# Kernel optimization log

Measured on AMD Instinct MI355X. Metric: run time of the kernel, lower is better.

The kernel has to match this reference:

```python
import jax, jax.numpy as jnp
import numpy as np

EMB_SCALE = 0.001  # embedding_scale when normalize=False


def setup_inputs() -> dict:
    key = jax.random.key(0)
    k1, k2 = jax.random.split(key)
    N, S, C, V, K = 8, 4096, 2, 128, 512
    x0 = jax.random.normal(k1, (N, S, C, V), dtype=jnp.float32)
    embedding = jax.random.normal(k2, (C, K, V), dtype=jnp.float32) * EMB_SCALE
    return {"x0": x0, "embedding": embedding}


def reference(x0, embedding):
    # normalize=False path: x = x0, embedding used as-is
    N, S, C, V = x0.shape
    K = embedding.shape[1]
    x = x0
    xf = x.reshape(N * S, C, V)  # (B, C, V), B = N*S tokens

    # (the ||x||^2 term is constant over k). Avoids materializing (B, C, K, V).
    dots = jnp.einsum('bcv,ckv->bck', xf, embedding)          # (B, C, K)
    e_sq = jnp.sum(embedding * embedding, axis=2)             # (C, K)
    dist2 = e_sq[None, :, :] - 2.0 * dots                     # (B, C, K)
    index = jnp.argmin(dist2, axis=2)                         # (B, C) int

    # Entropy of codebook usage (original divides by len(index) == B rows)
    B = N * S
    hist = jnp.bincount(index.reshape(-1), length=K).astype(jnp.float32)
    prob = hist / jnp.float32(B)
    entropy = -jnp.sum(jnp.where(hist > 0, prob * jnp.log(jnp.maximum(prob, 1e-30)), 0.0))

    # Gather: output[b, c] = embedding[c, index[b, c]]
    output = embedding[jnp.arange(C), index]                  # (B, C, V)
    output = output.reshape(N, S, C, V)

    out0 = jax.lax.stop_gradient(output - x) + x              # straight-through
    out1 = jnp.sum((jax.lax.stop_gradient(x) - output) ** 2, axis=3)  # (N,S,C)
    out2 = (jnp.sum((x - jax.lax.stop_gradient(output)) ** 2, axis=3)
            + jnp.sum((x - x0) ** 2, axis=3))                 # (N,S,C); (x-x0)==0 here
    return (out0, out1, out2, entropy)
```

## Files before the change

### kernel.cpp

```cpp
#include <hip/hip_runtime.h>
#include <math.h>

#define N_TOK    32768
#define C_CH     2
#define V_DIM    128
#define K_CODES  512
#define TPB      64

typedef short     bf16v8 __attribute__((ext_vector_type(8)));
typedef float     f32x4  __attribute__((ext_vector_type(4)));
typedef unsigned  u32x4  __attribute__((ext_vector_type(4)));

__device__ inline unsigned f2bf(float f) {
    unsigned u = __float_as_uint(f);
    return (u + 0x7FFFu + ((u >> 16) & 1u)) >> 16;
}
__device__ inline unsigned mapf(float d) {
    unsigned u = __float_as_uint(d);
    return ((int)u < 0) ? ~u : (u | 0x80000000u);
}

__device__ inline void pin4(u32x4& v) {
    unsigned a0 = v[0], a1 = v[1], a2 = v[2], a3 = v[3];
    asm volatile("" : "+v"(a0), "+v"(a1), "+v"(a2), "+v"(a3));
    v[0] = a0; v[1] = a1; v[2] = a2; v[3] = a3;
}

__global__ __launch_bounds__(64) void vq_prep(const float* __restrict__ emb,
                                              float* __restrict__ e_sq,
                                              unsigned int* __restrict__ hist,
                                              unsigned char* __restrict__ img) {
    const int row  = blockIdx.x;
    const int lane = threadIdx.x;
    const float a = emb[(size_t)row * V_DIM + lane];
    const float b = emb[(size_t)row * V_DIM + 64 + lane];
    float s = a * a + b * b;
#pragma unroll
    for (int off = 32; off; off >>= 1) s += __shfl_down(s, off);
    if (lane == 0) {
        e_sq[row] = s;
        if (row < K_CODES) hist[row] = 0u;
    }
    if (lane < 16) {
        const float* src = emb + (size_t)row * V_DIM + lane * 8;
        u32x4 val;
#pragma unroll
        for (int q = 0; q < 4; ++q)
            val[q] = f2bf(src[2 * q]) | (f2bf(src[2 * q + 1]) << 16);
        *reinterpret_cast<u32x4*>(img + ((size_t)row * 16 + lane) * 16) = val;
    }
}

__global__ __launch_bounds__(512, 2) void vq_main(const float* __restrict__ x0,
                                                  const float* __restrict__ emb,
                                                  const float* __restrict__ e_sq,
                                                  const unsigned char* __restrict__ img,
                                                  unsigned int* __restrict__ hist,
                                                  float* __restrict__ out0,
                                                  float* __restrict__ out1,
                                                  float* __restrict__ out2) {
    __shared__ unsigned long long best_s[TPB];

    const int c    = blockIdx.y;
    const int gt0  = blockIdx.x * TPB;
    const int t    = threadIdx.x;
    const int lane = t & 63;
    const int w    = t >> 6;
    const int l15  = lane & 15;
    const int l4   = lane >> 4;

    if (t < TPB) best_s[t] = ~0ull;

    u32x4 Bf[4][4];
    {
        const unsigned char* imgc = img + (size_t)(c * K_CODES + w * 64) * 256;
#pragma unroll
        for (int ct = 0; ct < 4; ++ct)
#pragma unroll
            for (int kk = 0; kk < 4; ++kk) {
                Bf[ct][kk] = *reinterpret_cast<const u32x4*>(
                    imgc + (size_t)(ct * 16 + l15) * 256 + (kk * 4 + l4) * 16);
                pin4(Bf[ct][kk]);
            }
    }
    float esq_r[4];
#pragma unroll
    for (int ct = 0; ct < 4; ++ct)
        esq_r[ct] = e_sq[c * K_CODES + w * 64 + ct * 16 + l15];

    __syncthreads();

    f32x4 raw[8];
    auto LOADX = [&](int tile_) {
        const float* xp = x0 + ((size_t)(gt0 + tile_ * 16 + l15) * C_CH + c) * V_DIM
                        + l4 * 8;
#pragma unroll
        for (int kk = 0; kk < 4; ++kk) {
            raw[2 * kk]     = *reinterpret_cast<const f32x4*>(xp + kk * 32);
            raw[2 * kk + 1] = *reinterpret_cast<const f32x4*>(xp + kk * 32 + 4);
        }
    };

    LOADX(0);
#pragma unroll
    for (int tile = 0; tile < 4; ++tile) {
        u32x4 A[4];
#pragma unroll
        for (int kk = 0; kk < 4; ++kk) {
            const f32x4 lo = raw[2 * kk], hi = raw[2 * kk + 1];
            u32x4 v;
            v[0] = f2bf(lo[0]) | (f2bf(lo[1]) << 16);
            v[1] = f2bf(lo[2]) | (f2bf(lo[3]) << 16);
            v[2] = f2bf(hi[0]) | (f2bf(hi[1]) << 16);
            v[3] = f2bf(hi[2]) | (f2bf(hi[3]) << 16);
            A[kk] = v;
        }

        if (tile < 3) LOADX(tile + 1);

        f32x4 acc[4];
#pragma unroll
        for (int ct = 0; ct < 4; ++ct) acc[ct] = (f32x4){0.f, 0.f, 0.f, 0.f};
#pragma unroll
        for (int kk = 0; kk < 4; ++kk)
#pragma unroll
            for (int ct = 0; ct < 4; ++ct)
                acc[ct] = __builtin_amdgcn_mfma_f32_16x16x32_bf16(
                    __builtin_bit_cast(bf16v8, A[kk]),
                    __builtin_bit_cast(bf16v8, Bf[ct][kk]), acc[ct], 0, 0, 0);

#pragma unroll
        for (int r = 0; r < 4; ++r) {
            unsigned long long m = ~0ull;
#pragma unroll
            for (int ct = 0; ct < 4; ++ct) {
                const float d = fmaf(-2.f, acc[ct][r], esq_r[ct]);
                const unsigned long long p =
                    ((unsigned long long)mapf(d) << 32)
                    | (unsigned)(w * 64 + ct * 16 + l15);
                if (p < m) m = p;
            }
#pragma unroll
            for (int s = 1; s < 16; s <<= 1) {
                const unsigned long long o = __shfl_xor(m, s);
                if (o < m) m = o;
            }
            if (l15 == 0)
                atomicMin(&best_s[tile * 16 + l4 * 4 + r], m);
        }
    }
    __syncthreads();

    const int g  = t >> 5;
    const int gl = t & 31;
#pragma unroll
    for (int i = 0; i < 4; ++i) {
        const int tok = i * 16 + g;
        const int k   = (int)(best_s[tok] & (unsigned long long)(K_CODES - 1));
        const size_t rowi = (size_t)(gt0 + tok) * C_CH + c;
        const f32x4 ev = *reinterpret_cast<const f32x4*>(
            emb + ((size_t)c * K_CODES + k) * V_DIM + gl * 4);
        const f32x4 xv = *reinterpret_cast<const f32x4*>(
            x0 + rowi * V_DIM + gl * 4);
        f32x4 ov;
        float s = 0.f;
#pragma unroll
        for (int z = 0; z < 4; ++z) {
            ov[z] = (ev[z] - xv[z]) + xv[z];
            const float dz = xv[z] - ev[z];
            s = fmaf(dz, dz, s);
        }
        *reinterpret_cast<f32x4*>(out0 + rowi * V_DIM + gl * 4) = ov;
#pragma unroll
        for (int m2 = 1; m2 <= 16; m2 <<= 1) s += __shfl_xor(s, m2);
        if (gl == 0) {
            out1[rowi] = s;
            out2[rowi] = s;
            atomicAdd(&hist[k], 1u);
        }
    }
}

__global__ __launch_bounds__(512) void vq_entropy(const unsigned int* __restrict__ hist,
                                                  float* __restrict__ ent) {
    const int t = threadIdx.x;
    float v = 0.f;
    const unsigned int h = hist[t];
    if (h > 0u) {
        const float p = (float)h * (1.0f / 32768.0f);
        v = p * logf(p);
    }
#pragma unroll
    for (int off = 32; off; off >>= 1) v += __shfl_down(v, off);
    __shared__ float s[8];
    if ((t & 63) == 0) s[t >> 6] = v;
    __syncthreads();
    if (t == 0) {
        float tot = 0.f;
#pragma unroll
        for (int i = 0; i < 8; ++i) tot += s[i];
        ent[0] = -tot;
    }
}

extern "C" void kernel_launch(void* const* d_in, const int* in_sizes, int n_in,
                              void* d_out, int out_size, void* d_ws, size_t ws_size,
                              hipStream_t stream) {
    const float* x0  = (const float*)d_in[0];
    const float* emb = (const float*)d_in[1];

    float*         e_sq = (float*)d_ws;
    unsigned int*  hist = (unsigned int*)((char*)d_ws + 4096);
    unsigned char* img  = (unsigned char*)d_ws + 8192;

    float* out0 = (float*)d_out;
    float* out1 = out0 + (size_t)N_TOK * C_CH * V_DIM;
    float* out2 = out1 + (size_t)N_TOK * C_CH;
    float* ent  = out2 + (size_t)N_TOK * C_CH;

    vq_prep<<<C_CH * K_CODES, 64, 0, stream>>>(emb, e_sq, hist, img);
    vq_main<<<dim3(N_TOK / TPB, C_CH), 512, 0, stream>>>(x0, emb, e_sq, img, hist,
                                                         out0, out1, out2);
    vq_entropy<<<1, K_CODES, 0, stream>>>(hist, ent);
}
```

Measured before the change: 88.40 us.

## Keep token tiles in registers and stream codebook fragments per wave

Restructures the distance kernel so each wave keeps two 16-token x tiles as bf16 fragments in registers and streams its 128 codes from the preconverted image in 16-code chunks. Previously each wave pinned 64 codes in registers and looped over four token tiles. The block shrinks from 64 tokens and 512 threads to 32 tokens and 256 threads, doubling the grid and dropping the two-blocks-per-CU launch bound. The intent is lower register pressure and more occupancy. The cost is reloading codebook fragments from global memory or L2 once per block, with less reuse per load.

Result: faster. 83.89 us (-5.1%).

```diff
diff --git a/kernel.cpp b/kernel.cpp
--- a/kernel.cpp
+++ b/kernel.cpp
@@ -5,7 +5,7 @@
 #define C_CH     2
 #define V_DIM    128
 #define K_CODES  512
-#define TPB      64
+#define TPB      32
 
 typedef short     bf16v8 __attribute__((ext_vector_type(8)));
 typedef float     f32x4  __attribute__((ext_vector_type(4)));
@@ -18,12 +18,6 @@
 __device__ inline unsigned mapf(float d) {
     unsigned u = __float_as_uint(d);
     return ((int)u < 0) ? ~u : (u | 0x80000000u);
-}
-
-__device__ inline void pin4(u32x4& v) {
-    unsigned a0 = v[0], a1 = v[1], a2 = v[2], a3 = v[3];
-    asm volatile("" : "+v"(a0), "+v"(a1), "+v"(a2), "+v"(a3));
-    v[0] = a0; v[1] = a1; v[2] = a2; v[3] = a3;
 }
 
 __global__ __launch_bounds__(64) void vq_prep(const float* __restrict__ emb,
@@ -51,14 +45,14 @@
     }
 }
 
-__global__ __launch_bounds__(512, 2) void vq_main(const float* __restrict__ x0,
-                                                  const float* __restrict__ emb,
-                                                  const float* __restrict__ e_sq,
-                                                  const unsigned char* __restrict__ img,
-                                                  unsigned int* __restrict__ hist,
-                                                  float* __restrict__ out0,
-                                                  float* __restrict__ out1,
-                                                  float* __restrict__ out2) {
+__global__ __launch_bounds__(256) void vq_main(const float* __restrict__ x0,
+                                               const float* __restrict__ emb,
+                                               const float* __restrict__ e_sq,
+                                               const unsigned char* __restrict__ img,
+                                               unsigned int* __restrict__ hist,
+                                               float* __restrict__ out0,
+                                               float* __restrict__ out1,
+                                               float* __restrict__ out2) {
     __shared__ unsigned long long best_s[TPB];
 
     const int c    = blockIdx.y;
@@ -71,82 +65,99 @@
 
     if (t < TPB) best_s[t] = ~0ull;
 
-    u32x4 Bf[4][4];
-    {
-        const unsigned char* imgc = img + (size_t)(c * K_CODES + w * 64) * 256;
-#pragma unroll
-        for (int ct = 0; ct < 4; ++ct)
-#pragma unroll
-            for (int kk = 0; kk < 4; ++kk) {
-                Bf[ct][kk] = *reinterpret_cast<const u32x4*>(
-                    imgc + (size_t)(ct * 16 + l15) * 256 + (kk * 4 + l4) * 16);
-                pin4(Bf[ct][kk]);
-            }
-    }
-    float esq_r[4];
-#pragma unroll
-    for (int ct = 0; ct < 4; ++ct)
-        esq_r[ct] = e_sq[c * K_CODES + w * 64 + ct * 16 + l15];
+    u32x4 A0[4], A1[4];
+#pragma unroll
+    for (int kk = 0; kk < 4; ++kk) {
+        const float* xp0 = x0 + ((size_t)(gt0 + l15) * C_CH + c) * V_DIM
+                         + kk * 32 + l4 * 8;
+        const f32x4 lo0 = *reinterpret_cast<const f32x4*>(xp0);
+        const f32x4 hi0 = *reinterpret_cast<const f32x4*>(xp0 + 4);
+        u32x4 v;
+        v[0] = f2bf(lo0[0]) | (f2bf(lo0[1]) << 16);
+        v[1] = f2bf(lo0[2]) | (f2bf(lo0[3]) << 16);
+        v[2] = f2bf(hi0[0]) | (f2bf(hi0[1]) << 16);
+        v[3] = f2bf(hi0[2]) | (f2bf(hi0[3]) << 16);
+        A0[kk] = v;
+    }
+#pragma unroll
+    for (int kk = 0; kk < 4; ++kk) {
+        const float* xp1 = x0 + ((size_t)(gt0 + 16 + l15) * C_CH + c) * V_DIM
+                         + kk * 32 + l4 * 8;
+        const f32x4 lo1 = *reinterpret_cast<const f32x4*>(xp1);
+        const f32x4 hi1 = *reinterpret_cast<const f32x4*>(xp1 + 4);
+        u32x4 v;
+        v[0] = f2bf(lo1[0]) | (f2bf(lo1[1]) << 16);
+        v[1] = f2bf(lo1[2]) | (f2bf(lo1[3]) << 16);
+        v[2] = f2bf(hi1[0]) | (f2bf(hi1[1]) << 16);
+        v[3] = f2bf(hi1[2]) | (f2bf(hi1[3]) << 16);
+        A1[kk] = v;
+    }
+
+    float esq_r[8];
+#pragma unroll
+    for (int j = 0; j < 8; ++j)
+        esq_r[j] = e_sq[c * K_CODES + w * 128 + j * 16 + l15];
 
     __syncthreads();
 
-    f32x4 raw[8];
-    auto LOADX = [&](int tile_) {
-        const float* xp = x0 + ((size_t)(gt0 + tile_ * 16 + l15) * C_CH + c) * V_DIM
-                        + l4 * 8;
-#pragma unroll
-        for (int kk = 0; kk < 4; ++kk) {
-            raw[2 * kk]     = *reinterpret_cast<const f32x4*>(xp + kk * 32);
-            raw[2 * kk + 1] = *reinterpret_cast<const f32x4*>(xp + kk * 32 + 4);
-        }
-    };
-
-    LOADX(0);
-#pragma unroll
-    for (int tile = 0; tile < 4; ++tile) {
-        u32x4 A[4];
-#pragma unroll
-        for (int kk = 0; kk < 4; ++kk) {
-            const f32x4 lo = raw[2 * kk], hi = raw[2 * kk + 1];
-            u32x4 v;
-            v[0] = f2bf(lo[0]) | (f2bf(lo[1]) << 16);
-            v[1] = f2bf(lo[2]) | (f2bf(lo[3]) << 16);
-            v[2] = f2bf(hi[0]) | (f2bf(hi[1]) << 16);
-            v[3] = f2bf(hi[2]) | (f2bf(hi[3]) << 16);
-            A[kk] = v;
-        }
-
-        if (tile < 3) LOADX(tile + 1);
-
-        f32x4 acc[4];
-#pragma unroll
-        for (int ct = 0; ct < 4; ++ct) acc[ct] = (f32x4){0.f, 0.f, 0.f, 0.f};
-#pragma unroll
-        for (int kk = 0; kk < 4; ++kk)
-#pragma unroll
-            for (int ct = 0; ct < 4; ++ct)
-                acc[ct] = __builtin_amdgcn_mfma_f32_16x16x32_bf16(
-                    __builtin_bit_cast(bf16v8, A[kk]),
-                    __builtin_bit_cast(bf16v8, Bf[ct][kk]), acc[ct], 0, 0, 0);
+    unsigned long long pk0[4], pk1[4];
+#pragma unroll
+    for (int r = 0; r < 4; ++r) { pk0[r] = ~0ull; pk1[r] = ~0ull; }
+
+#pragma unroll
+    for (int j = 0; j < 8; ++j) {
+        const int code = w * 128 + j * 16 + l15;
+        const unsigned char* bp = img + ((size_t)(c * K_CODES + code) * 16) * 16;
+        const u32x4 B0 = *reinterpret_cast<const u32x4*>(bp + (l4)      * 16);
+        const u32x4 B1 = *reinterpret_cast<const u32x4*>(bp + (4 + l4)  * 16);
+        const u32x4 B2 = *reinterpret_cast<const u32x4*>(bp + (8 + l4)  * 16);
+        const u32x4 B3 = *reinterpret_cast<const u32x4*>(bp + (12 + l4) * 16);
+
+        f32x4 a0 = {0.f, 0.f, 0.f, 0.f};
+        f32x4 a1 = {0.f, 0.f, 0.f, 0.f};
+        a0 = __builtin_amdgcn_mfma_f32_16x16x32_bf16(
+            __builtin_bit_cast(bf16v8, A0[0]), __builtin_bit_cast(bf16v8, B0), a0, 0, 0, 0);
+        a1 = __builtin_amdgcn_mfma_f32_16x16x32_bf16(
+            __builtin_bit_cast(bf16v8, A1[0]), __builtin_bit_cast(bf16v8, B0), a1, 0, 0, 0);
+        a0 = __builtin_amdgcn_mfma_f32_16x16x32_bf16(
+            __builtin_bit_cast(bf16v8, A0[1]), __builtin_bit_cast(bf16v8, B1), a0, 0, 0, 0);
+        a1 = __builtin_amdgcn_mfma_f32_16x16x32_bf16(
+            __builtin_bit_cast(bf16v8, A1[1]), __builtin_bit_cast(bf16v8, B1), a1, 0, 0, 0);
+        a0 = __builtin_amdgcn_mfma_f32_16x16x32_bf16(
+            __builtin_bit_cast(bf16v8, A0[2]), __builtin_bit_cast(bf16v8, B2), a0, 0, 0, 0);
+        a1 = __builtin_amdgcn_mfma_f32_16x16x32_bf16(
+            __builtin_bit_cast(bf16v8, A1[2]), __builtin_bit_cast(bf16v8, B2), a1, 0, 0, 0);
+        a0 = __builtin_amdgcn_mfma_f32_16x16x32_bf16(
+            __builtin_bit_cast(bf16v8, A0[3]), __builtin_bit_cast(bf16v8, B3), a0, 0, 0, 0);
+        a1 = __builtin_amdgcn_mfma_f32_16x16x32_bf16(
+            __builtin_bit_cast(bf16v8, A1[3]), __builtin_bit_cast(bf16v8, B3), a1, 0, 0, 0);
 
 #pragma unroll
         for (int r = 0; r < 4; ++r) {
-            unsigned long long m = ~0ull;
-#pragma unroll
-            for (int ct = 0; ct < 4; ++ct) {
-                const float d = fmaf(-2.f, acc[ct][r], esq_r[ct]);
-                const unsigned long long p =
-                    ((unsigned long long)mapf(d) << 32)
-                    | (unsigned)(w * 64 + ct * 16 + l15);
-                if (p < m) m = p;
-            }
-#pragma unroll
-            for (int s = 1; s < 16; s <<= 1) {
-                const unsigned long long o = __shfl_xor(m, s);
-                if (o < m) m = o;
-            }
-            if (l15 == 0)
-                atomicMin(&best_s[tile * 16 + l4 * 4 + r], m);
+            const float d0 = fmaf(-2.f, a0[r], esq_r[j]);
+            const unsigned long long p0 =
+                ((unsigned long long)mapf(d0) << 32) | (unsigned)code;
+            if (p0 < pk0[r]) pk0[r] = p0;
+            const float d1 = fmaf(-2.f, a1[r], esq_r[j]);
+            const unsigned long long p1 =
+                ((unsigned long long)mapf(d1) << 32) | (unsigned)code;
+            if (p1 < pk1[r]) pk1[r] = p1;
+        }
+    }
+
+#pragma unroll
+    for (int r = 0; r < 4; ++r) {
+        unsigned long long m0 = pk0[r], m1 = pk1[r];
+#pragma unroll
+        for (int s = 1; s < 16; s <<= 1) {
+            const unsigned long long o0 = __shfl_xor(m0, s);
+            if (o0 < m0) m0 = o0;
+            const unsigned long long o1 = __shfl_xor(m1, s);
+            if (o1 < m1) m1 = o1;
+        }
+        if (l15 == 0) {
+            atomicMin(&best_s[l4 * 4 + r], m0);
+            atomicMin(&best_s[16 + l4 * 4 + r], m1);
         }
     }
     __syncthreads();
@@ -155,7 +166,7 @@
     const int gl = t & 31;
 #pragma unroll
     for (int i = 0; i < 4; ++i) {
-        const int tok = i * 16 + g;
+        const int tok = i * 8 + g;
         const int k   = (int)(best_s[tok] & (unsigned long long)(K_CODES - 1));
         const size_t rowi = (size_t)(gt0 + tok) * C_CH + c;
         const f32x4 ev = *reinterpret_cast<const f32x4*>(
@@ -219,7 +230,7 @@
     float* ent  = out2 + (size_t)N_TOK * C_CH;
 
     vq_prep<<<C_CH * K_CODES, 64, 0, stream>>>(emb, e_sq, hist, img);
-    vq_main<<<dim3(N_TOK / TPB, C_CH), 512, 0, stream>>>(x0, emb, e_sq, img, hist,
+    vq_main<<<dim3(N_TOK / TPB, C_CH), 256, 0, stream>>>(x0, emb, e_sq, img, hist,
                                                          out0, out1, out2);
     vq_entropy<<<1, K_CODES, 0, stream>>>(hist, ent);
 }
```

## Restructure main kernel to stream codebook per wave and fuse entropy via last-block

Applied to the files above, without the earlier changes.

Each of four waves now owns a 16-token tile and loops over all 512 codes, streaming bf16 codebook fragments from global/L2 each iteration instead of holding a 64-code slice in registers across four token tiles. Block size drops to 256 threads and e_sq is staged in shared memory. The separate entropy kernel is removed; the last block to finish, detected with an atomic counter, computes the entropy. This cuts one launch and register pressure, but adds repeated codebook reads from cache and a serialized tail in the final block.

After: 212.4 us. 2.4x slower.

```diff
diff --git a/kernel.cpp b/kernel.cpp
--- a/kernel.cpp
+++ b/kernel.cpp
@@ -6,6 +6,7 @@
 #define V_DIM    128
 #define K_CODES  512
 #define TPB      64
+#define NBLOCKS  (N_TOK / TPB * C_CH)
 
 typedef short     bf16v8 __attribute__((ext_vector_type(8)));
 typedef float     f32x4  __attribute__((ext_vector_type(4)));
@@ -20,15 +21,10 @@
     return ((int)u < 0) ? ~u : (u | 0x80000000u);
 }
 
-__device__ inline void pin4(u32x4& v) {
-    unsigned a0 = v[0], a1 = v[1], a2 = v[2], a3 = v[3];
-    asm volatile("" : "+v"(a0), "+v"(a1), "+v"(a2), "+v"(a3));
-    v[0] = a0; v[1] = a1; v[2] = a2; v[3] = a3;
-}
-
 __global__ __launch_bounds__(64) void vq_prep(const float* __restrict__ emb,
                                               float* __restrict__ e_sq,
                                               unsigned int* __restrict__ hist,
+                                              unsigned int* __restrict__ done,
                                               unsigned char* __restrict__ img) {
     const int row  = blockIdx.x;
     const int lane = threadIdx.x;
@@ -40,6 +36,7 @@
     if (lane == 0) {
         e_sq[row] = s;
         if (row < K_CODES) hist[row] = 0u;
+        if (row == 0) *done = 0u;
     }
     if (lane < 16) {
         const float* src = emb + (size_t)row * V_DIM + lane * 8;
@@ -51,15 +48,20 @@
     }
 }
 
-__global__ __launch_bounds__(512, 2) void vq_main(const float* __restrict__ x0,
-                                                  const float* __restrict__ emb,
-                                                  const float* __restrict__ e_sq,
-                                                  const unsigned char* __restrict__ img,
-                                                  unsigned int* __restrict__ hist,
-                                                  float* __restrict__ out0,
-                                                  float* __restrict__ out1,
-                                                  float* __restrict__ out2) {
+__global__ __launch_bounds__(256) void vq_main(const float* __restrict__ x0,
+                                               const float* __restrict__ emb,
+                                               const float* __restrict__ e_sq,
+                                               const unsigned char* __restrict__ img,
+                                               unsigned int* __restrict__ hist,
+                                               unsigned int* __restrict__ done,
+                                               float* __restrict__ out0,
+                                               float* __restrict__ out1,
+                                               float* __restrict__ out2,
+                                               float* __restrict__ ent) {
     __shared__ unsigned long long best_s[TPB];
+    __shared__ float esq_s[K_CODES];
+    __shared__ float se[4];
+    __shared__ int last_s;
 
     const int c    = blockIdx.y;
     const int gt0  = blockIdx.x * TPB;
@@ -70,92 +72,74 @@
     const int l4   = lane >> 4;
 
     if (t < TPB) best_s[t] = ~0ull;
-
-    u32x4 Bf[4][4];
-    {
-        const unsigned char* imgc = img + (size_t)(c * K_CODES + w * 64) * 256;
-#pragma unroll
-        for (int ct = 0; ct < 4; ++ct)
-#pragma unroll
-            for (int kk = 0; kk < 4; ++kk) {
-                Bf[ct][kk] = *reinterpret_cast<const u32x4*>(
-                    imgc + (size_t)(ct * 16 + l15) * 256 + (kk * 4 + l4) * 16);
-                pin4(Bf[ct][kk]);
-            }
-    }
-    float esq_r[4];
-#pragma unroll
-    for (int ct = 0; ct < 4; ++ct)
-        esq_r[ct] = e_sq[c * K_CODES + w * 64 + ct * 16 + l15];
-
-    __syncthreads();
-
-    f32x4 raw[8];
-    auto LOADX = [&](int tile_) {
-        const float* xp = x0 + ((size_t)(gt0 + tile_ * 16 + l15) * C_CH + c) * V_DIM
-                        + l4 * 8;
-#pragma unroll
-        for (int kk = 0; kk < 4; ++kk) {
-            raw[2 * kk]     = *reinterpret_cast<const f32x4*>(xp + kk * 32);
-            raw[2 * kk + 1] = *reinterpret_cast<const f32x4*>(xp + kk * 32 + 4);
-        }
-    };
-
-    LOADX(0);
-#pragma unroll
-    for (int tile = 0; tile < 4; ++tile) {
-        u32x4 A[4];
-#pragma unroll
-        for (int kk = 0; kk < 4; ++kk) {
-            const f32x4 lo = raw[2 * kk], hi = raw[2 * kk + 1];
-            u32x4 v;
-            v[0] = f2bf(lo[0]) | (f2bf(lo[1]) << 16);
-            v[1] = f2bf(lo[2]) | (f2bf(lo[3]) << 16);
-            v[2] = f2bf(hi[0]) | (f2bf(hi[1]) << 16);
-            v[3] = f2bf(hi[2]) | (f2bf(hi[3]) << 16);
-            A[kk] = v;
-        }
-
-        if (tile < 3) LOADX(tile + 1);
-
-        f32x4 acc[4];
-#pragma unroll
-        for (int ct = 0; ct < 4; ++ct) acc[ct] = (f32x4){0.f, 0.f, 0.f, 0.f};
-#pragma unroll
-        for (int kk = 0; kk < 4; ++kk)
-#pragma unroll
-            for (int ct = 0; ct < 4; ++ct)
-                acc[ct] = __builtin_amdgcn_mfma_f32_16x16x32_bf16(
-                    __builtin_bit_cast(bf16v8, A[kk]),
-                    __builtin_bit_cast(bf16v8, Bf[ct][kk]), acc[ct], 0, 0, 0);
-
+    esq_s[t]       = e_sq[c * K_CODES + t];
+    esq_s[t + 256] = e_sq[c * K_CODES + t + 256];
+
+    u32x4 A[4];
+#pragma unroll
+    for (int kk = 0; kk < 4; ++kk) {
+        const float* xp = x0 + ((size_t)(gt0 + w * 16 + l15) * C_CH + c) * V_DIM
+                        + kk * 32 + l4 * 8;
+        const f32x4 lo = *reinterpret_cast<const f32x4*>(xp);
+        const f32x4 hi = *reinterpret_cast<const f32x4*>(xp + 4);
+        u32x4 v;
+        v[0] = f2bf(lo[0]) | (f2bf(lo[1]) << 16);
+        v[1] = f2bf(lo[2]) | (f2bf(lo[3]) << 16);
+        v[2] = f2bf(hi[0]) | (f2bf(hi[1]) << 16);
+        v[3] = f2bf(hi[2]) | (f2bf(hi[3]) << 16);
+        A[kk] = v;
+    }
+    __syncthreads();
+
+    unsigned long long pk[4] = {~0ull, ~0ull, ~0ull, ~0ull};
+    const unsigned char* imgc = img + (size_t)c * K_CODES * 256;
+
+#pragma unroll 4
+    for (int j = 0; j < 32; ++j) {
+        const int code = j * 16 + l15;
+        const unsigned char* bp = imgc + (size_t)code * 256 + l4 * 16;
+        const u32x4 B0 = *reinterpret_cast<const u32x4*>(bp);
+        const u32x4 B1 = *reinterpret_cast<const u32x4*>(bp + 64);
+        const u32x4 B2 = *reinterpret_cast<const u32x4*>(bp + 128);
+        const u32x4 B3 = *reinterpret_cast<const u32x4*>(bp + 192);
+
+        f32x4 acc = {0.f, 0.f, 0.f, 0.f};
+        acc = __builtin_amdgcn_mfma_f32_16x16x32_bf16(
+            __builtin_bit_cast(bf16v8, A[0]), __builtin_bit_cast(bf16v8, B0), acc, 0, 0, 0);
+        acc = __builtin_amdgcn_mfma_f32_16x16x32_bf16(
+            __builtin_bit_cast(bf16v8, A[1]), __builtin_bit_cast(bf16v8, B1), acc, 0, 0, 0);
+        acc = __builtin_amdgcn_mfma_f32_16x16x32_bf16(
+            __builtin_bit_cast(bf16v8, A[2]), __builtin_bit_cast(bf16v8, B2), acc, 0, 0, 0);
+        acc = __builtin_amdgcn_mfma_f32_16x16x32_bf16(
+            __builtin_bit_cast(bf16v8, A[3]), __builtin_bit_cast(bf16v8, B3), acc, 0, 0, 0);
+
+        const float esv = esq_s[code];
 #pragma unroll
         for (int r = 0; r < 4; ++r) {
-            unsigned long long m = ~0ull;
-#pragma unroll
-            for (int ct = 0; ct < 4; ++ct) {
-                const float d = fmaf(-2.f, acc[ct][r], esq_r[ct]);
-                const unsigned long long p =
-                    ((unsigned long long)mapf(d) << 32)
-                    | (unsigned)(w * 64 + ct * 16 + l15);
-                if (p < m) m = p;
-            }
-#pragma unroll
-            for (int s = 1; s < 16; s <<= 1) {
-                const unsigned long long o = __shfl_xor(m, s);
-                if (o < m) m = o;
-            }
-            if (l15 == 0)
-                atomicMin(&best_s[tile * 16 + l4 * 4 + r], m);
-        }
+            const float d = fmaf(-2.f, acc[r], esv);
+            const unsigned long long p =
+                ((unsigned long long)mapf(d) << 32) | (unsigned)code;
+            if (p < pk[r]) pk[r] = p;
+        }
+    }
+
+#pragma unroll
+    for (int r = 0; r < 4; ++r) {
+        unsigned long long m = pk[r];
+#pragma unroll
+        for (int s = 1; s < 16; s <<= 1) {
+            const unsigned long long o = __shfl_xor(m, s);
+            if (o < m) m = o;
+        }
+        if (l15 == 0) atomicMin(&best_s[w * 16 + l4 * 4 + r], m);
     }
     __syncthreads();
 
     const int g  = t >> 5;
     const int gl = t & 31;
 #pragma unroll
-    for (int i = 0; i < 4; ++i) {
-        const int tok = i * 16 + g;
+    for (int i = 0; i < 8; ++i) {
+        const int tok = i * 8 + g;
         const int k   = (int)(best_s[tok] & (unsigned long long)(K_CODES - 1));
         const size_t rowi = (size_t)(gt0 + tok) * C_CH + c;
         const f32x4 ev = *reinterpret_cast<const f32x4*>(
@@ -179,27 +163,27 @@
             atomicAdd(&hist[k], 1u);
         }
     }
-}
-
-__global__ __launch_bounds__(512) void vq_entropy(const unsigned int* __restrict__ hist,
-                                                  float* __restrict__ ent) {
-    const int t = threadIdx.x;
-    float v = 0.f;
-    const unsigned int h = hist[t];
-    if (h > 0u) {
-        const float p = (float)h * (1.0f / 32768.0f);
-        v = p * logf(p);
-    }
-#pragma unroll
-    for (int off = 32; off; off >>= 1) v += __shfl_down(v, off);
-    __shared__ float s[8];
-    if ((t & 63) == 0) s[t >> 6] = v;
-    __syncthreads();
-    if (t == 0) {
-        float tot = 0.f;
-#pragma unroll
-        for (int i = 0; i < 8; ++i) tot += s[i];
-        ent[0] = -tot;
+
+    __threadfence();
+    __syncthreads();
+    if (t == 0) last_s = (atomicAdd(done, 1u) == (unsigned)(NBLOCKS - 1));
+    __syncthreads();
+    if (last_s) {
+        __threadfence();
+        float v = 0.f;
+#pragma unroll
+        for (int b = t; b < K_CODES; b += 256) {
+            const unsigned h = atomicAdd(&hist[b], 0u);
+            if (h) {
+                const float p = (float)h * (1.0f / 32768.0f);
+                v = fmaf(p, logf(p), v);
+            }
+        }
+#pragma unroll
+        for (int off = 32; off; off >>= 1) v += __shfl_down(v, off);
+        if (lane == 0) se[w] = v;
+        __syncthreads();
+        if (t == 0) ent[0] = -(se[0] + se[1] + se[2] + se[3]);
     }
 }
 
@@ -211,6 +195,7 @@
 
     float*         e_sq = (float*)d_ws;
     unsigned int*  hist = (unsigned int*)((char*)d_ws + 4096);
+    unsigned int*  done = (unsigned int*)((char*)d_ws + 6144);
     unsigned char* img  = (unsigned char*)d_ws + 8192;
 
     float* out0 = (float*)d_out;
@@ -218,8 +203,8 @@
     float* out2 = out1 + (size_t)N_TOK * C_CH;
     float* ent  = out2 + (size_t)N_TOK * C_CH;
 
-    vq_prep<<<C_CH * K_CODES, 64, 0, stream>>>(emb, e_sq, hist, img);
-    vq_main<<<dim3(N_TOK / TPB, C_CH), 512, 0, stream>>>(x0, emb, e_sq, img, hist,
-                                                         out0, out1, out2);
-    vq_entropy<<<1, K_CODES, 0, stream>>>(hist, ent);
-}
+    vq_prep<<<C_CH * K_CODES, 64, 0, stream>>>(emb, e_sq, hist, done, img);
+    vq_main<<<dim3(N_TOK / TPB, C_CH), 256, 0, stream>>>(x0, emb, e_sq, img,
+                                                         hist, done,
+                                                         out0, out1, out2, ent);
+}
```
